# Optimization experiments

Measured on AMD Instinct MI355X. Metric: run time of the kernel, lower is better.

Reference implementation:

```python
import jax, jax.numpy as jnp
import numpy as np

B_SZ = 2
D_MODEL = 1024
H = 16
C = 8
BLK = 128
DK = 64
DV = 64
NCHUNK = 1024            # tokens per chunk (divisible by BLK)
T = C * (1 + NCHUNK)     # 8200: [g0, chunk0..., g1, chunk1..., ...]


def setup_inputs() -> dict:
    key = jax.random.key(0)
    k0, k1, k2, k3, k4 = jax.random.split(key, 5)
    s = 0.02
    x  = jax.random.normal(k0, (B_SZ, T, D_MODEL), dtype=jnp.float32)
    Wq = jax.random.normal(k1, (D_MODEL, H * DK), dtype=jnp.float32) * s
    Wk = jax.random.normal(k2, (D_MODEL, H * DK), dtype=jnp.float32) * s
    Wv = jax.random.normal(k3, (D_MODEL, H * DV), dtype=jnp.float32) * s
    Wo = jax.random.normal(k4, (H * DV, D_MODEL), dtype=jnp.float32) * s
    bo = jnp.zeros((D_MODEL,), dtype=jnp.float32)
    return {"x": x, "Wq": Wq, "Wk": Wk, "Wv": Wv, "Wo": Wo, "bo": bo}


def _local_sparse_3block(qf, kf, vf):
    # qf,kf: [BC, H, N, dk], vf: [BC, H, N, dv]; window = [left, current, right] blocks
    bc, h, n, dk = qf.shape
    dv = vf.shape[-1]
    nb = n // BLK
    q = qf.reshape(bc, h, nb, BLK, dk)
    k = kf.reshape(bc, h, nb, BLK, dk)
    v = vf.reshape(bc, h, nb, BLK, dv)
    zk = jnp.zeros((bc, h, 1, BLK, dk), qf.dtype)
    zv = jnp.zeros((bc, h, 1, BLK, dv), qf.dtype)
    kp = jnp.concatenate([zk, k, zk], axis=2)          # [bc,h,nb+2,B,dk]
    vp = jnp.concatenate([zv, v, zv], axis=2)
    k_win = jnp.concatenate([kp[:, :, 0:nb], kp[:, :, 1:nb + 1], kp[:, :, 2:nb + 2]], axis=3)  # [bc,h,nb,3B,dk]
    v_win = jnp.concatenate([vp[:, :, 0:nb], vp[:, :, 1:nb + 1], vp[:, :, 2:nb + 2]], axis=3)  # [bc,h,nb,3B,dv]
    scale = 1.0 / np.sqrt(dk).astype(np.float32)
    scores = jnp.einsum('bhnqd,bhnkd->bhnqk', q, k_win) * scale   # [bc,h,nb,B,3B]
    mask = np.zeros((nb, 3 * BLK), dtype=bool)
    mask[0, :BLK] = True           # first block: left padding invalid
    mask[-1, 2 * BLK:] = True      # last block: right padding invalid
    scores = jnp.where(jnp.asarray(mask)[None, None, :, None, :], -jnp.inf, scores)
    attn = jax.nn.softmax(scores, axis=-1)
    out = jnp.einsum('bhnqk,bhnkd->bhnqd', attn, v_win)
    return out.reshape(bc, h, n, dv)


def reference(x, Wq, Wk, Wv, Wo, bo):
    Bb, Tt, _ = x.shape
    q = (x @ Wq).reshape(Bb, Tt, H, DK).transpose(0, 2, 1, 3)  # [B,H,T,dk]
    k = (x @ Wk).reshape(Bb, Tt, H, DK).transpose(0, 2, 1, 3)
    v = (x @ Wv).reshape(Bb, Tt, H, DV).transpose(0, 2, 1, 3)
    stride = NCHUNK + 1
    g_idx = jnp.arange(C) * stride
    gq = q[:, :, g_idx]  # [B,H,C,dk]
    gk = k[:, :, g_idx]
    gv = v[:, :, g_idx]  # [B,H,C,dv]
    local_idx = ((g_idx + 1)[:, None] + jnp.arange(NCHUNK)[None, :]).reshape(-1)
    qx = q[:, :, local_idx].reshape(Bb, H, C, NCHUNK, DK)
    kx = k[:, :, local_idx].reshape(Bb, H, C, NCHUNK, DK)
    vx = v[:, :, local_idx].reshape(Bb, H, C, NCHUNK, DV)
    # local 3-block attention per chunk
    q_flat = qx.transpose(0, 2, 1, 3, 4).reshape(Bb * C, H, NCHUNK, DK)
    k_flat = kx.transpose(0, 2, 1, 3, 4).reshape(Bb * C, H, NCHUNK, DK)
    v_flat = vx.transpose(0, 2, 1, 3, 4).reshape(Bb * C, H, NCHUNK, DV)
    out_local = _local_sparse_3block(q_flat, k_flat, v_flat)
    out_local = out_local.reshape(Bb, C, H, NCHUNK, DV).transpose(0, 2, 1, 3, 4)  # [B,H,C,Nchunk,dv]
    # each local token additionally receives its chunk's global value directly
    out_chunks = out_local + gv[:, :, :, None, :]
    # global tokens attend over all globals + own chunk's locals (joint softmax, fp32)
    scale = 1.0 / np.sqrt(DK).astype(np.float32)
    scores_gg = jnp.einsum('bhcd,bhed->bhce', gq, gk) * scale      # [B,H,C,C]
    scores_gl = jnp.einsum('bhcd,bhcnd->bhcn', gq, kx) * scale     # [B,H,C,Nchunk]
    attn = jax.nn.softmax(jnp.concatenate([scores_gg, scores_gl], axis=-1), axis=-1)
    a_gg, a_gl = attn[..., :C], attn[..., C:]
    out_g = (jnp.einsum('bhce,bhed->bhcd', a_gg, gv)
             + jnp.einsum('bhcn,bhcnd->bhcd', a_gl, vx))           # [B,H,C,dv]
    out_inter = jnp.concatenate([out_g[:, :, :, None, :], out_chunks], axis=3)  # [B,H,C,1+Nchunk,dv]
    out = out_inter.reshape(Bb, H, Tt, DV).transpose(0, 2, 1, 3).reshape(Bb, Tt, H * DV)
    return out @ Wo + bo
```

## Files before the change

### kernel.cpp

```cpp
#include <hip/hip_runtime.h>

typedef __bf16 bf16x8 __attribute__((ext_vector_type(8)));
typedef float  f32x4  __attribute__((ext_vector_type(4)));
typedef unsigned short u16x8 __attribute__((ext_vector_type(8)));
typedef unsigned short u16x4 __attribute__((ext_vector_type(4)));

#define T_TOK   8200
#define M_TOK   16400
#define QKV_LD  3072
#define DM      1024

#define AS1CU const __attribute__((address_space(1))) unsigned int*
#define AS3U  __attribute__((address_space(3))) unsigned int*
#define GLDS16(g, s) __builtin_amdgcn_global_load_lds((AS1CU)(g), (AS3U)(s), 16, 0, 0)

__device__ __forceinline__ unsigned short f2bf(float f){
  union { float f; unsigned u; } x; x.f = f;
  unsigned r = (x.u + 0x7fffu + ((x.u >> 16) & 1u)) >> 16;
  return (unsigned short)r;
}
__device__ __forceinline__ float bf2f(unsigned short u){
  union { unsigned u; float f; } x; x.u = ((unsigned)u) << 16;
  return x.f;
}

__global__ void k_cvt(const float* __restrict__ in, unsigned short* __restrict__ out, long n4){
  long i = (long)blockIdx.x * blockDim.x + threadIdx.x;
  long stride = (long)gridDim.x * blockDim.x;
  for (long e = i; e < n4; e += stride){
    float4 v = ((const float4*)in)[e];
    u16x4 o; o[0]=f2bf(v.x); o[1]=f2bf(v.y); o[2]=f2bf(v.z); o[3]=f2bf(v.w);
    ((u16x4*)out)[e] = o;
  }
}

__global__ __launch_bounds__(256) void k_wT(const float* __restrict__ W, unsigned short* __restrict__ Wt,
                                            int Kd, int Nd){
  __shared__ float t[64][65];
  int tk0 = blockIdx.x * 64, tn0 = blockIdx.y * 64;
  int tid = threadIdx.x;
#pragma unroll
  for (int i = 0; i < 4; i++){
    int ch = tid + i*256; int kr = ch >> 4, n4 = (ch & 15) * 4;
    float4 v = *(const float4*)(W + (size_t)(tk0+kr)*Nd + tn0 + n4);
    t[kr][n4+0]=v.x; t[kr][n4+1]=v.y; t[kr][n4+2]=v.z; t[kr][n4+3]=v.w;
  }
  __syncthreads();
#pragma unroll
  for (int i = 0; i < 4; i++){
    int ch = tid + i*256; int nr = ch >> 4, k4 = (ch & 15) * 4;
    u16x4 o;
#pragma unroll
    for (int e = 0; e < 4; e++) o[e] = f2bf(t[k4+e][nr]);
    *(u16x4*)(Wt + (size_t)(tn0+nr)*Kd + tk0 + k4) = o;
  }
}

__global__ __launch_bounds__(256,2) void k_gemm(const unsigned short* __restrict__ A,
                                                const unsigned short* __restrict__ Bt,
                                                const float* __restrict__ bias,
                                                void* __restrict__ Cout,
                                                int M, int K, int ldc, int bf16out, int gn){
  __shared__ unsigned short As[128][64];
  __shared__ unsigned short Bs[128][64];
  int tid = threadIdx.x, l = tid & 63, w = tid >> 6;
  int li = l & 15, lh = l >> 4;
  int nwg = gridDim.x;
  int wg = (blockIdx.x & 7) * (nwg >> 3) + (blockIdx.x >> 3);
  int m0 = (wg / gn) * 128, n0 = (wg % gn) * 128;
  int wm = (w & 1) * 64, wn = (w >> 1) * 64;
  int lr = l >> 3, lc = l & 7;
  int lsw = li & 7;

  f32x4 acc[4][4];
#pragma unroll
  for (int a = 0; a < 4; a++)
#pragma unroll
    for (int b = 0; b < 4; b++) acc[a][b] = 0.f;

  for (int kt = 0; kt < K; kt += 64){
    __syncthreads();
#pragma unroll
    for (int i = 0; i < 4; i++){
      int r = w*32 + i*8 + lr;
      int colsw = (lc ^ (r & 7)) * 8;
      int rga = m0 + r; if (rga >= M) rga = M - 1;
      GLDS16(A  + (size_t)rga     *K + kt + colsw, &As[w*32 + i*8][0]);
      GLDS16(Bt + (size_t)(n0 + r)*K + kt + colsw, &Bs[w*32 + i*8][0]);
    }
    __syncthreads();
#pragma unroll
    for (int ks = 0; ks < 2; ks++){
      bf16x8 af[4], bfr[4];
#pragma unroll
      for (int mt = 0; mt < 4; mt++)
        af[mt] = *(const bf16x8*)&As[wm + mt*16 + li][((ks*4 + lh) ^ lsw) * 8];
#pragma unroll
      for (int nt = 0; nt < 4; nt++)
        bfr[nt] = *(const bf16x8*)&Bs[wn + nt*16 + li][((ks*4 + lh) ^ lsw) * 8];
#pragma unroll
      for (int mt = 0; mt < 4; mt++)
#pragma unroll
        for (int nt = 0; nt < 4; nt++)
          acc[mt][nt] = __builtin_amdgcn_mfma_f32_16x16x32_bf16(af[mt], bfr[nt], acc[mt][nt], 0, 0, 0);
    }
  }
#pragma unroll
  for (int mt = 0; mt < 4; mt++)
#pragma unroll
    for (int nt = 0; nt < 4; nt++)
#pragma unroll
      for (int r = 0; r < 4; r++){
        int row = m0 + wm + mt*16 + lh*4 + r;
        int col = n0 + wn + nt*16 + li;
        if (row < M){
          float v = acc[mt][nt][r] + (bias ? bias[col] : 0.f);
          if (bf16out) ((unsigned short*)Cout)[(size_t)row*ldc + col] = f2bf(v);
          else         ((float*)Cout)[(size_t)row*ldc + col] = v;
        }
      }
}

__global__ __launch_bounds__(256,2) void k_local(const unsigned short* __restrict__ qkv,
                                                 unsigned short* __restrict__ att){
  __shared__ unsigned short Ks[128][64];
  __shared__ unsigned short Vt[64][136];
  __shared__ unsigned short PbV[9216];

  int tid = threadIdx.x, l = tid & 63, w = tid >> 6;
  int li = l & 15, lh = l >> 4;
  int lr = l >> 3, lc = l & 7;
  int lsw = li & 7;
  int wg = (blockIdx.x & 7) * 256 + (blockIdx.x >> 3);
  int blk = wg & 7, c = (wg >> 3) & 7, h = (wg >> 6) & 15, b = wg >> 10;
  size_t bT = (size_t)b * T_TOK;
  int tokq0 = c*1025 + 1 + blk*128;

  bf16x8 aq[2][2];
#pragma unroll
  for (int tr = 0; tr < 2; tr++)
#pragma unroll
    for (int ks = 0; ks < 2; ks++)
      aq[tr][ks] = *(const bf16x8*)(qkv + (bT + tokq0 + w*32 + tr*16 + li)*QKV_LD + h*64 + ks*32 + lh*8);

  float mrun[2][4], lrun[2][4];
  f32x4 oacc[2][4];
#pragma unroll
  for (int tr = 0; tr < 2; tr++)
#pragma unroll
    for (int r = 0; r < 4; r++){ mrun[tr][r] = -3e38f; lrun[tr][r] = 0.f; }
#pragma unroll
  for (int tr = 0; tr < 2; tr++)
#pragma unroll
    for (int ct = 0; ct < 4; ct++) oacc[tr][ct] = 0.f;

  for (int kb = blk-1; kb <= blk+1; ++kb){
    if ((unsigned)kb > 7u) continue;
    int tokk0 = c*1025 + 1 + kb*128;
    __syncthreads();
#pragma unroll
    for (int i = 0; i < 4; i++){
      int r = w*32 + i*8 + lr;
      int colk = (lc ^ (r & 7)) * 8;
      GLDS16(qkv + (bT + tokk0 + r)*QKV_LD + 1024 + h*64 + colk, &Ks[w*32 + i*8][0]);
    }
#pragma unroll
    for (int i = 0; i < 4; i++){
      int ch = tid + i*256; int r = ch >> 3, g = ch & 7;
      u16x8 vv = *(const u16x8*)(qkv + (bT + tokk0 + r)*QKV_LD + 2048 + h*64 + g*8);
      int gs = g ^ ((r >> 3) & 7);
      *(u16x8*)&PbV[r*72 + gs*8] = vv;
    }
    __syncthreads();
#pragma unroll
    for (int dd = 0; dd < 16; dd++){
      int d = w*16 + dd; int gd = d >> 3, dl = d & 7;
      int r0 = 2*l;
      int gsw = (gd ^ ((r0 >> 3) & 7)) * 8 + dl;
      unsigned lo = PbV[ r0   *72 + gsw];
      unsigned hi = PbV[(r0+1)*72 + gsw];
      *(unsigned*)&Vt[d][2*l] = lo | (hi << 16);
    }
    __syncthreads();
    bf16x8 vf[4][4];
#pragma unroll
    for (int ct = 0; ct < 4; ct++)
#pragma unroll
      for (int ks = 0; ks < 4; ks++)
        vf[ct][ks] = *(const bf16x8*)&Vt[ct*16 + li][ks*32 + lh*8];

    f32x4 s2[2][8];
#pragma unroll
    for (int tr = 0; tr < 2; tr++)
#pragma unroll
      for (int ct = 0; ct < 8; ct++) s2[tr][ct] = 0.f;
#pragma unroll
    for (int ct = 0; ct < 8; ct++)
#pragma unroll
      for (int ks = 0; ks < 2; ks++){
        bf16x8 kf = *(const bf16x8*)&Ks[ct*16 + li][((ks*4 + lh) ^ lsw) * 8];
        s2[0][ct] = __builtin_amdgcn_mfma_f32_16x16x32_bf16(aq[0][ks], kf, s2[0][ct], 0, 0, 0);
        s2[1][ct] = __builtin_amdgcn_mfma_f32_16x16x32_bf16(aq[1][ks], kf, s2[1][ct], 0, 0, 0);
      }

    for (int tr = 0; tr < 2; tr++){
      float rmax[4] = {-3e38f,-3e38f,-3e38f,-3e38f};
#pragma unroll
      for (int ct = 0; ct < 8; ct++)
#pragma unroll
        for (int r = 0; r < 4; r++){
          float v = s2[tr][ct][r] * 0.125f; s2[tr][ct][r] = v;
          rmax[r] = fmaxf(rmax[r], v);
        }
#pragma unroll
      for (int r = 0; r < 4; r++)
#pragma unroll
        for (int mk = 1; mk < 16; mk <<= 1)
          rmax[r] = fmaxf(rmax[r], __shfl_xor(rmax[r], mk));
      float alpha[4], rsum[4] = {0.f,0.f,0.f,0.f};
#pragma unroll
      for (int r = 0; r < 4; r++){
        float mn = fmaxf(mrun[tr][r], rmax[r]);
        alpha[r] = __expf(mrun[tr][r] - mn);
        mrun[tr][r] = mn;
      }
#pragma unroll
      for (int ct = 0; ct < 8; ct++)
#pragma unroll
        for (int r = 0; r < 4; r++){
          float p = __expf(s2[tr][ct][r] - mrun[tr][r]);
          s2[tr][ct][r] = p; rsum[r] += p;
        }
#pragma unroll
      for (int r = 0; r < 4; r++)
#pragma unroll
        for (int mk = 1; mk < 16; mk <<= 1)
          rsum[r] += __shfl_xor(rsum[r], mk);
#pragma unroll
      for (int r = 0; r < 4; r++) lrun[tr][r] = lrun[tr][r]*alpha[r] + rsum[r];
#pragma unroll
      for (int ct = 0; ct < 4; ct++)
#pragma unroll
        for (int r = 0; r < 4; r++) oacc[tr][ct][r] *= alpha[r];
#pragma unroll
      for (int ct = 0; ct < 8; ct++)
#pragma unroll
        for (int r = 0; r < 4; r++)
          PbV[w*2176 + (lh*4 + r)*136 + ct*16 + li] = f2bf(s2[tr][ct][r]);
      bf16x8 pa[4];
#pragma unroll
      for (int ks = 0; ks < 4; ks++)
        pa[ks] = *(const bf16x8*)&PbV[w*2176 + li*136 + ks*32 + lh*8];
#pragma unroll
      for (int ct = 0; ct < 4; ct++)
#pragma unroll
        for (int ks = 0; ks < 4; ks++)
          oacc[tr][ct] = __builtin_amdgcn_mfma_f32_16x16x32_bf16(pa[ks], vf[ct][ks], oacc[tr][ct], 0, 0, 0);
    }
  }

  float gvv[4];
#pragma unroll
  for (int ct = 0; ct < 4; ct++)
    gvv[ct] = bf2f(qkv[(bT + c*1025)*QKV_LD + 2048 + h*64 + ct*16 + li]);
#pragma unroll
  for (int tr = 0; tr < 2; tr++)
#pragma unroll
    for (int ct = 0; ct < 4; ct++)
#pragma unroll
      for (int r = 0; r < 4; r++){
        int row = w*32 + tr*16 + lh*4 + r;
        float v = oacc[tr][ct][r] / lrun[tr][r] + gvv[ct];
        att[(bT + tokq0 + row)*DM + h*64 + ct*16 + li] = f2bf(v);
      }
}

__global__ __launch_bounds__(256) void k_global(const unsigned short* __restrict__ qkv,
                                                unsigned short* __restrict__ att){
  __shared__ float sc[1032];
  __shared__ float red[256];
  __shared__ float gq_s[64];
  int tid = threadIdx.x, bid = blockIdx.x;
  int c = bid & 7, h = (bid >> 3) & 15, b = bid >> 7;
  size_t bT = (size_t)b * T_TOK;
  size_t grow = bT + (size_t)c*1025;
  if (tid < 64) gq_s[tid] = bf2f(qkv[grow*QKV_LD + h*64 + tid]);
  __syncthreads();
  float lmax = -3e38f;
  for (int idx = tid; idx < 1032; idx += 256){
    size_t krow = (idx < 8) ? (bT + (size_t)idx*1025) : (bT + (size_t)c*1025 + 1 + (idx - 8));
    const unsigned short* kp = qkv + krow*QKV_LD + 1024 + h*64;
    float s = 0.f;
#pragma unroll
    for (int d0 = 0; d0 < 64; d0 += 8){
      u16x8 kv = *(const u16x8*)(kp + d0);
#pragma unroll
      for (int e = 0; e < 8; e++) s += gq_s[d0+e] * bf2f(kv[e]);
    }
    s *= 0.125f;
    sc[idx] = s;
    lmax = fmaxf(lmax, s);
  }
  red[tid] = lmax; __syncthreads();
  for (int st = 128; st > 0; st >>= 1){ if (tid < st) red[tid] = fmaxf(red[tid], red[tid+st]); __syncthreads(); }
  float m = red[0]; __syncthreads();
  float lsum = 0.f;
  for (int idx = tid; idx < 1032; idx += 256){
    float p = __expf(sc[idx] - m); sc[idx] = p; lsum += p;
  }
  red[tid] = lsum; __syncthreads();
  for (int st = 128; st > 0; st >>= 1){ if (tid < st) red[tid] += red[tid+st]; __syncthreads(); }
  float denom = red[0]; __syncthreads();
  int d = tid & 63, part = tid >> 6;
  float acc = 0.f;
  for (int idx = part; idx < 1032; idx += 4){
    size_t krow = (idx < 8) ? (bT + (size_t)idx*1025) : (bT + (size_t)c*1025 + 1 + (idx - 8));
    acc += sc[idx] * bf2f(qkv[krow*QKV_LD + 2048 + h*64 + d]);
  }
  red[tid] = acc; __syncthreads();
  if (tid < 64){
    float o = (red[tid] + red[tid+64] + red[tid+128] + red[tid+192]) / denom;
    att[grow*DM + h*64 + tid] = f2bf(o);
  }
}

extern "C" void kernel_launch(void* const* d_in, const int* in_sizes, int n_in,
                              void* d_out, int out_size, void* d_ws, size_t ws_size,
                              hipStream_t stream) {
  const float* x  = (const float*)d_in[0];
  const float* Wq = (const float*)d_in[1];
  const float* Wk = (const float*)d_in[2];
  const float* Wv = (const float*)d_in[3];
  const float* Wo = (const float*)d_in[4];
  const float* bo = (const float*)d_in[5];
  float* out = (float*)d_out;

  unsigned short* xb    = (unsigned short*)d_ws;
  unsigned short* wqkvt = xb    + (size_t)M_TOK * 1024;
  unsigned short* wot   = wqkvt + (size_t)3072 * 1024;
  unsigned short* qkv   = wot   + (size_t)1024 * 1024;
  unsigned short* att   = qkv   + (size_t)M_TOK * QKV_LD;

  long n4 = (long)M_TOK * 1024 / 4;
  k_cvt<<<2048, 256, 0, stream>>>(x, xb, n4);
  k_wT<<<dim3(16,16), 256, 0, stream>>>(Wq, wqkvt,                        1024, 1024);
  k_wT<<<dim3(16,16), 256, 0, stream>>>(Wk, wqkvt + (size_t)1024*1024,    1024, 1024);
  k_wT<<<dim3(16,16), 256, 0, stream>>>(Wv, wqkvt + (size_t)2048*1024,    1024, 1024);
  k_wT<<<dim3(16,16), 256, 0, stream>>>(Wo, wot,                          1024, 1024);
  k_gemm<<<dim3(129*24), 256, 0, stream>>>(xb, wqkvt, (const float*)nullptr, (void*)qkv,
                                           M_TOK, 1024, QKV_LD, 1, 24);
  k_local<<<2048, 256, 0, stream>>>(qkv, att);
  k_global<<<256, 256, 0, stream>>>(qkv, att);
  k_gemm<<<dim3(129*8), 256, 0, stream>>>(att, wot, bo, (void*)out,
                                          M_TOK, 1024, DM, 0, 8);
}
```

Baseline: 367.9 us.

## Merge weight transposes, raise local-attention occupancy, reload V fragments per MFMA

Four separate weight transpose launches are merged into one 3D-grid kernel to cut launch overhead. The local attention kernel raises its launch-bounds occupancy hint from 2 to 3 and stops holding all 16 V fragments in registers, reading them from LDS right before each MFMA. This lowers register pressure but adds repeated LDS reads inside the tr loop. The bf16 rounding helper is also switched to the HIP library conversion.

```diff
diff --git a/kernel.cpp b/kernel.cpp
--- a/kernel.cpp
+++ b/kernel.cpp
@@ -1,4 +1,5 @@
 #include <hip/hip_runtime.h>
+#include <hip/hip_bf16.h>
 
 typedef __bf16 bf16x8 __attribute__((ext_vector_type(8)));
 typedef float  f32x4  __attribute__((ext_vector_type(4)));
@@ -15,9 +16,8 @@
 #define GLDS16(g, s) __builtin_amdgcn_global_load_lds((AS1CU)(g), (AS3U)(s), 16, 0, 0)
 
 __device__ __forceinline__ unsigned short f2bf(float f){
-  union { float f; unsigned u; } x; x.f = f;
-  unsigned r = (x.u + 0x7fffu + ((x.u >> 16) & 1u)) >> 16;
-  return (unsigned short)r;
+  __hip_bfloat16 h = __float2bfloat16(f);
+  return *reinterpret_cast<unsigned short*>(&h);
 }
 __device__ __forceinline__ float bf2f(unsigned short u){
   union { unsigned u; float f; } x; x.u = ((unsigned)u) << 16;
@@ -34,15 +34,22 @@
   }
 }
 
-__global__ __launch_bounds__(256) void k_wT(const float* __restrict__ W, unsigned short* __restrict__ Wt,
-                                            int Kd, int Nd){
+__global__ __launch_bounds__(256) void k_wT4(const float* __restrict__ Wq, const float* __restrict__ Wk,
+                                             const float* __restrict__ Wv, const float* __restrict__ Wo,
+                                             unsigned short* __restrict__ wqkvt, unsigned short* __restrict__ wot){
   __shared__ float t[64][65];
+  const float* W; unsigned short* Wt;
+  int z = blockIdx.z;
+  if      (z == 0){ W = Wq; Wt = wqkvt; }
+  else if (z == 1){ W = Wk; Wt = wqkvt + (size_t)1024*1024; }
+  else if (z == 2){ W = Wv; Wt = wqkvt + (size_t)2048*1024; }
+  else            { W = Wo; Wt = wot; }
   int tk0 = blockIdx.x * 64, tn0 = blockIdx.y * 64;
   int tid = threadIdx.x;
 #pragma unroll
   for (int i = 0; i < 4; i++){
     int ch = tid + i*256; int kr = ch >> 4, n4 = (ch & 15) * 4;
-    float4 v = *(const float4*)(W + (size_t)(tk0+kr)*Nd + tn0 + n4);
+    float4 v = *(const float4*)(W + (size_t)(tk0+kr)*1024 + tn0 + n4);
     t[kr][n4+0]=v.x; t[kr][n4+1]=v.y; t[kr][n4+2]=v.z; t[kr][n4+3]=v.w;
   }
   __syncthreads();
@@ -52,7 +59,7 @@
     u16x4 o;
 #pragma unroll
     for (int e = 0; e < 4; e++) o[e] = f2bf(t[k4+e][nr]);
-    *(u16x4*)(Wt + (size_t)(tn0+nr)*Kd + tk0 + k4) = o;
+    *(u16x4*)(Wt + (size_t)(tn0+nr)*1024 + tk0 + k4) = o;
   }
 }
 
@@ -121,7 +128,7 @@
       }
 }
 
-__global__ __launch_bounds__(256,2) void k_local(const unsigned short* __restrict__ qkv,
+__global__ __launch_bounds__(256,3) void k_local(const unsigned short* __restrict__ qkv,
                                                  unsigned short* __restrict__ att){
   __shared__ unsigned short Ks[128][64];
   __shared__ unsigned short Vt[64][136];
@@ -182,12 +189,6 @@
       *(unsigned*)&Vt[d][2*l] = lo | (hi << 16);
     }
     __syncthreads();
-    bf16x8 vf[4][4];
-#pragma unroll
-    for (int ct = 0; ct < 4; ct++)
-#pragma unroll
-      for (int ks = 0; ks < 4; ks++)
-        vf[ct][ks] = *(const bf16x8*)&Vt[ct*16 + li][ks*32 + lh*8];
 
     f32x4 s2[2][8];
 #pragma unroll
@@ -254,8 +255,10 @@
 #pragma unroll
       for (int ct = 0; ct < 4; ct++)
 #pragma unroll
-        for (int ks = 0; ks < 4; ks++)
-          oacc[tr][ct] = __builtin_amdgcn_mfma_f32_16x16x32_bf16(pa[ks], vf[ct][ks], oacc[tr][ct], 0, 0, 0);
+        for (int ks = 0; ks < 4; ks++){
+          bf16x8 vfr = *(const bf16x8*)&Vt[ct*16 + li][ks*32 + lh*8];
+          oacc[tr][ct] = __builtin_amdgcn_mfma_f32_16x16x32_bf16(pa[ks], vfr, oacc[tr][ct], 0, 0, 0);
+        }
     }
   }
 
@@ -343,10 +346,7 @@
 
   long n4 = (long)M_TOK * 1024 / 4;
   k_cvt<<<2048, 256, 0, stream>>>(x, xb, n4);
-  k_wT<<<dim3(16,16), 256, 0, stream>>>(Wq, wqkvt,                        1024, 1024);
-  k_wT<<<dim3(16,16), 256, 0, stream>>>(Wk, wqkvt + (size_t)1024*1024,    1024, 1024);
-  k_wT<<<dim3(16,16), 256, 0, stream>>>(Wv, wqkvt + (size_t)2048*1024,    1024, 1024);
-  k_wT<<<dim3(16,16), 256, 0, stream>>>(Wo, wot,                          1024, 1024);
+  k_wT4<<<dim3(16,16,4), 256, 0, stream>>>(Wq, Wk, Wv, Wo, wqkvt, wot);
   k_gemm<<<dim3(129*24), 256, 0, stream>>>(xb, wqkvt, (const float*)nullptr, (void*)qkv,
                                            M_TOK, 1024, QKV_LD, 1, 24);
   k_local<<<2048, 256, 0, stream>>>(qkv, att);
```

After: 370.8 us. About the same (+0.8%).
